# Kernel optimization log

Hardware: AMD Instinct MI355X
Metric: run time of the kernel (lower is better)

## Reference

```python
import jax, jax.numpy as jnp
import numpy as np

D_MODEL = 1024
HIDDEN = 64
N_STEPS = 6
T0, T1 = 0.0, 1.0


def setup_inputs() -> dict:
    key = jax.random.key(0)
    kx, k1, k2, k3, k4 = jax.random.split(key, 5)
    # PyTorch nn.Linear default init: U(-1/sqrt(fan_in), 1/sqrt(fan_in))
    s1 = 1.0 / np.sqrt(D_MODEL + 1)
    s2 = 1.0 / np.sqrt(HIDDEN)
    return {
        "x": jax.random.normal(kx, (8, 2048, D_MODEL), dtype=jnp.float32),
        "W1": jax.random.uniform(k1, (D_MODEL + 1, HIDDEN), jnp.float32, -s1, s1),
        "b1": jax.random.uniform(k2, (HIDDEN,), jnp.float32, -s1, s1),
        "W2": jax.random.uniform(k3, (HIDDEN, D_MODEL), jnp.float32, -s2, s2),
        "b2": jax.random.uniform(k4, (D_MODEL,), jnp.float32, -s2, s2),
    }


def _dynamics(t, z, W1, b1, W2, b2):
    # Equivalent to concat([z, t*ones], -1) @ W1: split the last row of W1
    # (the time channel) so we avoid materializing the concat.
    h = jnp.tanh(jnp.einsum("btd,dh->bth", z, W1[:-1]) + t * W1[-1] + b1)
    return jnp.einsum("bth,hd->btd", h, W2) + b2


def reference(x, W1, b1, W2, b2):
    h = (T1 - T0) / N_STEPS  # step size
    ts = T0 + h * jnp.arange(N_STEPS, dtype=x.dtype)

    def rk4_step(z, t):
        k1 = _dynamics(t, z, W1, b1, W2, b2)
        k2 = _dynamics(t + h / 2, z + (h / 2) * k1, W1, b1, W2, b2)
        k3 = _dynamics(t + h / 2, z + (h / 2) * k2, W1, b1, W2, b2)
        k4 = _dynamics(t + h, z + h * k3, W1, b1, W2, b2)
        z_next = z + (h / 6) * (k1 + 2 * k2 + 2 * k3 + k4)
        return z_next, None

    z_T, _ = jax.lax.scan(rk4_step, x, ts)
    return z_T
```

## Files before the change

### kernel.cpp

```cpp
#include <hip/hip_runtime.h>
#include <hip/hip_bf16.h>

#define DM 1024
#define HID 64
#define NSTEP 6
#define RSTEP (1.0f/6.0f)

using short8  = __attribute__((ext_vector_type(8))) short;
using short4v = __attribute__((ext_vector_type(4))) short;
using f32x4   = __attribute__((ext_vector_type(4))) float;

#define WS_W1P 0
#define WS_W2P 131072
#define WS_GP  262144
#define WS_U   270336

#define L_H0 0
#define L_H1 2304
#define L_HB 4608
#define L_B2 6912
#define LDS_TOTAL 11008
#define HP 144

#define BAR() asm volatile("s_waitcnt lgkmcnt(0)\n\ts_barrier" ::: "memory")

__device__ __forceinline__ short f2bf(float f) {
    __hip_bfloat16 h = __float2bfloat16(f);
    short s;
    __builtin_memcpy(&s, &h, 2);
    return s;
}
__device__ __forceinline__ float ftanh(float x) {
    x = fminf(fmaxf(x, -10.f), 10.f);
    float e = __expf(2.f * x);
    return __fdividef(e - 1.f, e + 1.f);
}

__global__ void k_prep(const float* __restrict__ W1, const float* __restrict__ W2,
                       const float* __restrict__ b2,
                       short* __restrict__ W1P, short* __restrict__ W2P,
                       short* __restrict__ GP, float* __restrict__ U) {
    __shared__ float red[4][64];
    int b = blockIdx.x;
    int t = threadIdx.x;
    int l = t & 63, q4 = t >> 6;
    if (b < 128) {
        if (t < 64) {
            int kk = b >> 2, c = b & 3;
            int col = c * 16 + (l & 15);
            int kb = kk * 32 + ((l >> 4) << 3);
            short8 v;
            #pragma unroll
            for (int i = 0; i < 8; ++i) v[i] = f2bf(W1[(kb + i) * HID + col]);
            *(short8*)(W1P + (((kk * 4 + c) * 64) + l) * 8) = v;
        }
    } else if (b < 256) {
        if (t < 64) {
            int bb = b - 128;
            int kk2 = bb >> 6, ct = bb & 63;
            int col = ct * 16 + (l & 15);
            int kb = kk2 * 32 + ((l >> 4) << 3);
            short8 v;
            #pragma unroll
            for (int i = 0; i < 8; ++i) v[i] = f2bf(W2[(kb + i) * DM + col]);
            *(short8*)(W2P + (((kk2 * 64 + ct) * 64) + l) * 8) = v;
        }
    } else if (b < 320) {
        int j = b - 256;
        float acc = 0.f;
        #pragma unroll 8
        for (int d = q4 * 256; d < q4 * 256 + 256; ++d)
            acc += W2[j * DM + d] * W1[d * HID + l];
        red[q4][l] = acc;
        __syncthreads();
        if (t < 64) {
            float a = red[0][l] + red[1][l] + red[2][l] + red[3][l];
            int kk = j >> 5, lk = (j >> 3) & 3, ii = j & 7, c = l >> 4, lo = l & 15;
            GP[(((kk * 4 + c) * 64) + lk * 16 + lo) * 8 + ii] = f2bf(a);
        }
    } else {
        float acc = 0.f;
        #pragma unroll 8
        for (int d = q4 * 256; d < q4 * 256 + 256; ++d)
            acc += b2[d] * W1[d * HID + l];
        red[q4][l] = acc;
        __syncthreads();
        if (t < 64) U[l] = red[0][l] + red[1][l] + red[2][l] + red[3][l];
    }
}

__global__ __launch_bounds__(256) __attribute__((amdgpu_waves_per_eu(2, 4)))
void k_ode(
        const float* __restrict__ X, const float* __restrict__ W1,
        const float* __restrict__ b1, const float* __restrict__ b2,
        const short* __restrict__ W1P, const short* __restrict__ W2P,
        const short* __restrict__ GP, const float* __restrict__ U,
        float* __restrict__ OUT) {
    extern __shared__ char smem[];
    const int t = threadIdx.x;
    const int lane = t & 63;
    const int w = t >> 6;
    const int hq = lane >> 4;
    const int l15 = lane & 15;
    const int hcol0 = w * 16 + hq * 4;
    const size_t row0 = (size_t)blockIdx.x * 16;

    *(f32x4*)(smem + L_B2 + t * 16) = *(const f32x4*)(b2 + t * 4);

    f32x4 u4   = *(const f32x4*)(U + hcol0);
    f32x4 b14  = *(const f32x4*)(b1 + hcol0);
    f32x4 w1t4 = *(const f32x4*)(W1 + DM * HID + hcol0);
    short8 gf0 = *(const short8*)(GP + (w * 64 + lane) * 8);
    short8 gf1 = *(const short8*)(GP + ((4 + w) * 64 + lane) * 8);

    f32x4 sz;
    {
        const float* xrow = X + (row0 + l15) * DM;
        const short8* wp = (const short8*)W1P + (w * 64 + lane);
        f32x4 a0 = (f32x4){0.f, 0.f, 0.f, 0.f};
        f32x4 a1 = (f32x4){0.f, 0.f, 0.f, 0.f};
        #pragma unroll 4
        for (int kk = 0; kk < 32; kk += 2) {
            const float* xp = xrow + (kk << 5) + (hq << 3);
            f32x4 lo0 = *(const f32x4*)(xp);
            f32x4 hi0 = *(const f32x4*)(xp + 4);
            f32x4 lo1 = *(const f32x4*)(xp + 32);
            f32x4 hi1 = *(const f32x4*)(xp + 36);
            short8 zf0, zf1;
            #pragma unroll
            for (int j = 0; j < 4; ++j) {
                zf0[j] = f2bf(lo0[j]); zf0[4 + j] = f2bf(hi0[j]);
                zf1[j] = f2bf(lo1[j]); zf1[4 + j] = f2bf(hi1[j]);
            }
            a0 = __builtin_amdgcn_mfma_f32_16x16x32_bf16(wp[kk * 256],       zf0, a0, 0, 0, 0);
            a1 = __builtin_amdgcn_mfma_f32_16x16x32_bf16(wp[(kk + 1) * 256], zf1, a1, 0, 0, 0);
        }
        sz = a0 + a1;
    }

    f32x4 ssum = (f32x4){0.f, 0.f, 0.f, 0.f};

    for (int s = 0; s < NSTEP; ++s) {
        const float tcur = RSTEP * (float)s;

        f32x4 hsum;
        {
            short4v hc;
            #pragma unroll
            for (int j = 0; j < 4; ++j) {
                float T = sz[j] + tcur * w1t4[j] + b14[j];
                float h = ftanh(T);
                hsum[j] = h;
                hc[j] = f2bf(h);
            }
            *(short4v*)(smem + L_H0 + l15 * HP + hcol0 * 2) = hc;
        }
        BAR();

        #pragma unroll
        for (int st = 0; st < 3; ++st) {
            const float c_i = (st == 2) ? RSTEP : (0.5f * RSTEP);
            const float t_i = tcur + ((st == 2) ? RSTEP : (0.5f * RSTEP));
            const float w_i = (st == 2) ? 1.f : 2.f;
            const int rbuf = (st & 1) ? L_H1 : L_H0;
            const int wbuf = (st & 1) ? L_H0 : L_H1;

            short8 hf0 = *(const short8*)(smem + rbuf + l15 * HP + (hq << 4));
            short8 hf1 = *(const short8*)(smem + rbuf + l15 * HP + 64 + (hq << 4));
            f32x4 dd = (f32x4){0.f, 0.f, 0.f, 0.f};
            dd = __builtin_amdgcn_mfma_f32_16x16x32_bf16(gf0, hf0, dd, 0, 0, 0);
            dd = __builtin_amdgcn_mfma_f32_16x16x32_bf16(gf1, hf1, dd, 0, 0, 0);
            short4v hc;
            #pragma unroll
            for (int j = 0; j < 4; ++j) {
                float T = sz[j] + c_i * (dd[j] + u4[j]) + t_i * w1t4[j] + b14[j];
                float h = ftanh(T);
                hsum[j] += w_i * h;
                hc[j] = f2bf(h);
            }
            if (st < 2) {
                *(short4v*)(smem + wbuf + l15 * HP + hcol0 * 2) = hc;
            } else {
                short4v hb4;
                #pragma unroll
                for (int j = 0; j < 4; ++j) {
                    ssum[j] += hsum[j] * (RSTEP / 6.f);
                    hb4[j] = (s < NSTEP - 1) ? f2bf(hsum[j] * (RSTEP / 6.f))
                                             : f2bf(ssum[j]);
                }
                *(short4v*)(smem + L_HB + l15 * HP + hcol0 * 2) = hb4;
            }
            BAR();
        }

        if (s < NSTEP - 1) {
            short8 hb0 = *(const short8*)(smem + L_HB + l15 * HP + (hq << 4));
            short8 hb1 = *(const short8*)(smem + L_HB + l15 * HP + 64 + (hq << 4));
            f32x4 d = (f32x4){0.f, 0.f, 0.f, 0.f};
            d = __builtin_amdgcn_mfma_f32_16x16x32_bf16(gf0, hb0, d, 0, 0, 0);
            d = __builtin_amdgcn_mfma_f32_16x16x32_bf16(gf1, hb1, d, 0, 0, 0);
            #pragma unroll
            for (int j = 0; j < 4; ++j)
                sz[j] += d[j] + RSTEP * u4[j];
        }
    }

    {
        short8 sb0 = *(const short8*)(smem + L_HB + l15 * HP + (hq << 4));
        short8 sb1 = *(const short8*)(smem + L_HB + l15 * HP + 64 + (hq << 4));
        const short8* w2p8 = (const short8*)W2P;
        const float* xrow = X + (row0 + l15) * DM + w * 256;
        float* orow = OUT + (row0 + l15) * DM + w * 256;
        #pragma unroll 4
        for (int q = 0; q < 16; ++q) {
            int ct = w * 16 + q;
            short8 wa = w2p8[ct * 64 + lane];
            short8 wb = w2p8[(64 + ct) * 64 + lane];
            f32x4 p = (f32x4){0.f, 0.f, 0.f, 0.f};
            p = __builtin_amdgcn_mfma_f32_16x16x32_bf16(wa, sb0, p, 0, 0, 0);
            p = __builtin_amdgcn_mfma_f32_16x16x32_bf16(wb, sb1, p, 0, 0, 0);
            f32x4 b2v = *(const f32x4*)(smem + L_B2 + (ct * 16 + hq * 4) * 4);
            f32x4 xv  = *(const f32x4*)(xrow + q * 16 + hq * 4);
            f32x4 nv;
            #pragma unroll
            for (int j = 0; j < 4; ++j)
                nv[j] = xv[j] + p[j] + b2v[j];
            *(f32x4*)(orow + q * 16 + hq * 4) = nv;
        }
    }
}

extern "C" void kernel_launch(void* const* d_in, const int* in_sizes, int n_in,
                              void* d_out, int out_size, void* d_ws, size_t ws_size,
                              hipStream_t stream) {
    (void)in_sizes; (void)n_in; (void)out_size; (void)ws_size;
    const float* X  = (const float*)d_in[0];
    const float* W1 = (const float*)d_in[1];
    const float* b1 = (const float*)d_in[2];
    const float* W2 = (const float*)d_in[3];
    const float* b2 = (const float*)d_in[4];
    float* OUT = (float*)d_out;
    short* W1P = (short*)((char*)d_ws + WS_W1P);
    short* W2P = (short*)((char*)d_ws + WS_W2P);
    short* GP  = (short*)((char*)d_ws + WS_GP);
    float* U   = (float*)((char*)d_ws + WS_U);

    k_prep<<<321, 256, 0, stream>>>(W1, W2, b2, W1P, W2P, GP, U);
    k_ode<<<1024, 256, LDS_TOTAL, stream>>>(X, W1, b1, b2, W1P, W2P, GP, U, OUT);
}
```

Before: 78.51 us.

## Use single-wave blocks to drop barriers and precompute per-stage bias vectors

Shrinks each ODE block from four waves to one. The single wave now owns all 64 hidden columns across four MFMA tiles, so the workgroup barriers between RK4 stages reduce to LDS waitcnt fences and one LDS buffer replaces the two ping-pong buffers plus the separate sum buffer. The prep kernel also precomputes per-step, per-stage constant vectors (b1 + t*w1t + c*u) and h*u, which removes per-element arithmetic from the inner loop. In exchange, each wave holds more register state and does four times the serial MFMA and global-load work, and only 1024 single-wave blocks remain to fill the device. That may reduce latency hiding.

```diff
diff --git a/kernel.cpp b/kernel.cpp
--- a/kernel.cpp
+++ b/kernel.cpp
@@ -14,15 +14,16 @@
 #define WS_W2P 131072
 #define WS_GP  262144
 #define WS_U   270336
-
-#define L_H0 0
-#define L_H1 2304
-#define L_HB 4608
-#define L_B2 6912
-#define LDS_TOTAL 11008
+#define WS_VST 270592
+#define WS_HU  276736
+
+#define L_H   0
+#define L_VST 2304
+#define L_HU  8448
+#define LDS_TOTAL 8704
 #define HP 144
 
-#define BAR() asm volatile("s_waitcnt lgkmcnt(0)\n\ts_barrier" ::: "memory")
+#define FENCE() asm volatile("s_waitcnt lgkmcnt(0)" ::: "memory")
 
 __device__ __forceinline__ short f2bf(float f) {
     __hip_bfloat16 h = __float2bfloat16(f);
@@ -37,9 +38,10 @@
 }
 
 __global__ void k_prep(const float* __restrict__ W1, const float* __restrict__ W2,
-                       const float* __restrict__ b2,
+                       const float* __restrict__ b1, const float* __restrict__ b2,
                        short* __restrict__ W1P, short* __restrict__ W2P,
-                       short* __restrict__ GP, float* __restrict__ U) {
+                       short* __restrict__ GP, float* __restrict__ U,
+                       float* __restrict__ VST, float* __restrict__ HU) {
     __shared__ float red[4][64];
     int b = blockIdx.x;
     int t = threadIdx.x;
@@ -85,147 +87,158 @@
             acc += b2[d] * W1[d * HID + l];
         red[q4][l] = acc;
         __syncthreads();
-        if (t < 64) U[l] = red[0][l] + red[1][l] + red[2][l] + red[3][l];
-    }
-}
-
-__global__ __launch_bounds__(256) __attribute__((amdgpu_waves_per_eu(2, 4)))
+        if (t < 64) {
+            float uu = red[0][l] + red[1][l] + red[2][l] + red[3][l];
+            U[l] = uu;
+            HU[l] = RSTEP * uu;
+            float b1l = b1[l];
+            float wtl = W1[DM * HID + l];
+            #pragma unroll
+            for (int s6 = 0; s6 < 6; ++s6) {
+                float ts = RSTEP * (float)s6;
+                float tm = ts + 0.5f * RSTEP;
+                float vmid = b1l + tm * wtl + 0.5f * RSTEP * uu;
+                VST[(s6 * 4 + 0) * 64 + l] = b1l + ts * wtl;
+                VST[(s6 * 4 + 1) * 64 + l] = vmid;
+                VST[(s6 * 4 + 2) * 64 + l] = vmid;
+                VST[(s6 * 4 + 3) * 64 + l] = b1l + (ts + RSTEP) * wtl + RSTEP * uu;
+            }
+        }
+    }
+}
+
+__global__ __launch_bounds__(64) __attribute__((amdgpu_waves_per_eu(2, 4)))
 void k_ode(
-        const float* __restrict__ X, const float* __restrict__ W1,
-        const float* __restrict__ b1, const float* __restrict__ b2,
+        const float* __restrict__ X, const float* __restrict__ b2,
         const short* __restrict__ W1P, const short* __restrict__ W2P,
-        const short* __restrict__ GP, const float* __restrict__ U,
-        float* __restrict__ OUT) {
+        const short* __restrict__ GP, const float* __restrict__ VST,
+        const float* __restrict__ HU, float* __restrict__ OUT) {
     extern __shared__ char smem[];
-    const int t = threadIdx.x;
-    const int lane = t & 63;
-    const int w = t >> 6;
+    const int lane = threadIdx.x & 63;
     const int hq = lane >> 4;
     const int l15 = lane & 15;
-    const int hcol0 = w * 16 + hq * 4;
     const size_t row0 = (size_t)blockIdx.x * 16;
-
-    *(f32x4*)(smem + L_B2 + t * 16) = *(const f32x4*)(b2 + t * 4);
-
-    f32x4 u4   = *(const f32x4*)(U + hcol0);
-    f32x4 b14  = *(const f32x4*)(b1 + hcol0);
-    f32x4 w1t4 = *(const f32x4*)(W1 + DM * HID + hcol0);
-    short8 gf0 = *(const short8*)(GP + (w * 64 + lane) * 8);
-    short8 gf1 = *(const short8*)(GP + ((4 + w) * 64 + lane) * 8);
-
-    f32x4 sz;
+    const float* xrow = X + (row0 + l15) * DM;
+
+    #pragma unroll
+    for (int i = 0; i < 6; ++i)
+        *(f32x4*)(smem + L_VST + i * 1024 + lane * 16) =
+            *(const f32x4*)(VST + i * 256 + lane * 4);
+    if (lane < 16)
+        *(f32x4*)(smem + L_HU + lane * 16) = *(const f32x4*)(HU + lane * 4);
+
+    short8 gfr[2][4];
+    #pragma unroll
+    for (int k2 = 0; k2 < 2; ++k2)
+        #pragma unroll
+        for (int c = 0; c < 4; ++c)
+            gfr[k2][c] = *(const short8*)(GP + ((k2 * 4 + c) * 64 + lane) * 8);
+
+    f32x4 sz[4] = {(f32x4){0.f,0.f,0.f,0.f}, (f32x4){0.f,0.f,0.f,0.f},
+                   (f32x4){0.f,0.f,0.f,0.f}, (f32x4){0.f,0.f,0.f,0.f}};
     {
-        const float* xrow = X + (row0 + l15) * DM;
-        const short8* wp = (const short8*)W1P + (w * 64 + lane);
-        f32x4 a0 = (f32x4){0.f, 0.f, 0.f, 0.f};
-        f32x4 a1 = (f32x4){0.f, 0.f, 0.f, 0.f};
+        const short8* wp = (const short8*)W1P;
         #pragma unroll 4
-        for (int kk = 0; kk < 32; kk += 2) {
+        for (int kk = 0; kk < 32; ++kk) {
             const float* xp = xrow + (kk << 5) + (hq << 3);
-            f32x4 lo0 = *(const f32x4*)(xp);
-            f32x4 hi0 = *(const f32x4*)(xp + 4);
-            f32x4 lo1 = *(const f32x4*)(xp + 32);
-            f32x4 hi1 = *(const f32x4*)(xp + 36);
-            short8 zf0, zf1;
+            f32x4 lo = *(const f32x4*)(xp);
+            f32x4 hi = *(const f32x4*)(xp + 4);
+            short8 zf;
+            #pragma unroll
+            for (int j = 0; j < 4; ++j) { zf[j] = f2bf(lo[j]); zf[4 + j] = f2bf(hi[j]); }
+            #pragma unroll
+            for (int c = 0; c < 4; ++c)
+                sz[c] = __builtin_amdgcn_mfma_f32_16x16x32_bf16(
+                            wp[(kk * 4 + c) * 64 + lane], zf, sz[c], 0, 0, 0);
+        }
+    }
+
+    f32x4 ssum[4] = {(f32x4){0.f,0.f,0.f,0.f}, (f32x4){0.f,0.f,0.f,0.f},
+                     (f32x4){0.f,0.f,0.f,0.f}, (f32x4){0.f,0.f,0.f,0.f}};
+
+    for (int s = 0; s < NSTEP; ++s) {
+        f32x4 hsum[4];
+
+        #pragma unroll
+        for (int c = 0; c < 4; ++c) {
+            f32x4 vst = *(const f32x4*)(smem + L_VST + (s * 4 + 0) * 256 + c * 64 + (hq << 4));
+            short4v hc;
             #pragma unroll
             for (int j = 0; j < 4; ++j) {
-                zf0[j] = f2bf(lo0[j]); zf0[4 + j] = f2bf(hi0[j]);
-                zf1[j] = f2bf(lo1[j]); zf1[4 + j] = f2bf(hi1[j]);
-            }
-            a0 = __builtin_amdgcn_mfma_f32_16x16x32_bf16(wp[kk * 256],       zf0, a0, 0, 0, 0);
-            a1 = __builtin_amdgcn_mfma_f32_16x16x32_bf16(wp[(kk + 1) * 256], zf1, a1, 0, 0, 0);
-        }
-        sz = a0 + a1;
-    }
-
-    f32x4 ssum = (f32x4){0.f, 0.f, 0.f, 0.f};
-
-    for (int s = 0; s < NSTEP; ++s) {
-        const float tcur = RSTEP * (float)s;
-
-        f32x4 hsum;
-        {
-            short4v hc;
-            #pragma unroll
-            for (int j = 0; j < 4; ++j) {
-                float T = sz[j] + tcur * w1t4[j] + b14[j];
-                float h = ftanh(T);
-                hsum[j] = h;
+                float h = ftanh(sz[c][j] + vst[j]);
+                hsum[c][j] = h;
                 hc[j] = f2bf(h);
             }
-            *(short4v*)(smem + L_H0 + l15 * HP + hcol0 * 2) = hc;
-        }
-        BAR();
+            *(short4v*)(smem + L_H + l15 * HP + c * 32 + (hq << 3)) = hc;
+        }
+        FENCE();
 
         #pragma unroll
-        for (int st = 0; st < 3; ++st) {
-            const float c_i = (st == 2) ? RSTEP : (0.5f * RSTEP);
-            const float t_i = tcur + ((st == 2) ? RSTEP : (0.5f * RSTEP));
-            const float w_i = (st == 2) ? 1.f : 2.f;
-            const int rbuf = (st & 1) ? L_H1 : L_H0;
-            const int wbuf = (st & 1) ? L_H0 : L_H1;
-
-            short8 hf0 = *(const short8*)(smem + rbuf + l15 * HP + (hq << 4));
-            short8 hf1 = *(const short8*)(smem + rbuf + l15 * HP + 64 + (hq << 4));
-            f32x4 dd = (f32x4){0.f, 0.f, 0.f, 0.f};
-            dd = __builtin_amdgcn_mfma_f32_16x16x32_bf16(gf0, hf0, dd, 0, 0, 0);
-            dd = __builtin_amdgcn_mfma_f32_16x16x32_bf16(gf1, hf1, dd, 0, 0, 0);
-            short4v hc;
-            #pragma unroll
-            for (int j = 0; j < 4; ++j) {
-                float T = sz[j] + c_i * (dd[j] + u4[j]) + t_i * w1t4[j] + b14[j];
-                float h = ftanh(T);
-                hsum[j] += w_i * h;
-                hc[j] = f2bf(h);
-            }
-            if (st < 2) {
-                *(short4v*)(smem + wbuf + l15 * HP + hcol0 * 2) = hc;
-            } else {
-                short4v hb4;
+        for (int e = 1; e < 4; ++e) {
+            const float ce = (e == 3) ? RSTEP : (0.5f * RSTEP);
+            const float we = (e == 3) ? 1.f : 2.f;
+            short8 hf0 = *(const short8*)(smem + L_H + l15 * HP + (hq << 4));
+            short8 hf1 = *(const short8*)(smem + L_H + l15 * HP + 64 + (hq << 4));
+            #pragma unroll
+            for (int c = 0; c < 4; ++c) {
+                f32x4 dd = (f32x4){0.f, 0.f, 0.f, 0.f};
+                dd = __builtin_amdgcn_mfma_f32_16x16x32_bf16(gfr[0][c], hf0, dd, 0, 0, 0);
+                dd = __builtin_amdgcn_mfma_f32_16x16x32_bf16(gfr[1][c], hf1, dd, 0, 0, 0);
+                f32x4 vst = *(const f32x4*)(smem + L_VST + (s * 4 + e) * 256 + c * 64 + (hq << 4));
+                short4v hc;
                 #pragma unroll
                 for (int j = 0; j < 4; ++j) {
-                    ssum[j] += hsum[j] * (RSTEP / 6.f);
-                    hb4[j] = (s < NSTEP - 1) ? f2bf(hsum[j] * (RSTEP / 6.f))
-                                             : f2bf(ssum[j]);
+                    float h = ftanh(sz[c][j] + ce * dd[j] + vst[j]);
+                    hsum[c][j] += we * h;
+                    if (e < 3) {
+                        hc[j] = f2bf(h);
+                    } else {
+                        ssum[c][j] += hsum[c][j] * (RSTEP / 6.f);
+                        hc[j] = (s < NSTEP - 1) ? f2bf(hsum[c][j] * (RSTEP / 6.f))
+                                                : f2bf(ssum[c][j]);
+                    }
                 }
-                *(short4v*)(smem + L_HB + l15 * HP + hcol0 * 2) = hb4;
-            }
-            BAR();
+                *(short4v*)(smem + L_H + l15 * HP + c * 32 + (hq << 3)) = hc;
+            }
+            FENCE();
         }
 
         if (s < NSTEP - 1) {
-            short8 hb0 = *(const short8*)(smem + L_HB + l15 * HP + (hq << 4));
-            short8 hb1 = *(const short8*)(smem + L_HB + l15 * HP + 64 + (hq << 4));
-            f32x4 d = (f32x4){0.f, 0.f, 0.f, 0.f};
-            d = __builtin_amdgcn_mfma_f32_16x16x32_bf16(gf0, hb0, d, 0, 0, 0);
-            d = __builtin_amdgcn_mfma_f32_16x16x32_bf16(gf1, hb1, d, 0, 0, 0);
-            #pragma unroll
-            for (int j = 0; j < 4; ++j)
-                sz[j] += d[j] + RSTEP * u4[j];
+            short8 hb0 = *(const short8*)(smem + L_H + l15 * HP + (hq << 4));
+            short8 hb1 = *(const short8*)(smem + L_H + l15 * HP + 64 + (hq << 4));
+            #pragma unroll
+            for (int c = 0; c < 4; ++c) {
+                f32x4 d = (f32x4){0.f, 0.f, 0.f, 0.f};
+                d = __builtin_amdgcn_mfma_f32_16x16x32_bf16(gfr[0][c], hb0, d, 0, 0, 0);
+                d = __builtin_amdgcn_mfma_f32_16x16x32_bf16(gfr[1][c], hb1, d, 0, 0, 0);
+                f32x4 hu4 = *(const f32x4*)(smem + L_HU + c * 64 + (hq << 4));
+                #pragma unroll
+                for (int j = 0; j < 4; ++j)
+                    sz[c][j] += d[j] + hu4[j];
+            }
         }
     }
 
     {
-        short8 sb0 = *(const short8*)(smem + L_HB + l15 * HP + (hq << 4));
-        short8 sb1 = *(const short8*)(smem + L_HB + l15 * HP + 64 + (hq << 4));
+        short8 sb0 = *(const short8*)(smem + L_H + l15 * HP + (hq << 4));
+        short8 sb1 = *(const short8*)(smem + L_H + l15 * HP + 64 + (hq << 4));
         const short8* w2p8 = (const short8*)W2P;
-        const float* xrow = X + (row0 + l15) * DM + w * 256;
-        float* orow = OUT + (row0 + l15) * DM + w * 256;
+        float* orow = OUT + (row0 + l15) * DM;
         #pragma unroll 4
-        for (int q = 0; q < 16; ++q) {
-            int ct = w * 16 + q;
+        for (int ct = 0; ct < 64; ++ct) {
             short8 wa = w2p8[ct * 64 + lane];
             short8 wb = w2p8[(64 + ct) * 64 + lane];
             f32x4 p = (f32x4){0.f, 0.f, 0.f, 0.f};
             p = __builtin_amdgcn_mfma_f32_16x16x32_bf16(wa, sb0, p, 0, 0, 0);
             p = __builtin_amdgcn_mfma_f32_16x16x32_bf16(wb, sb1, p, 0, 0, 0);
-            f32x4 b2v = *(const f32x4*)(smem + L_B2 + (ct * 16 + hq * 4) * 4);
-            f32x4 xv  = *(const f32x4*)(xrow + q * 16 + hq * 4);
+            int col = ct * 16 + (hq << 2);
+            f32x4 xv  = *(const f32x4*)(xrow + col);
+            f32x4 b2v = *(const f32x4*)(b2 + col);
             f32x4 nv;
             #pragma unroll
             for (int j = 0; j < 4; ++j)
                 nv[j] = xv[j] + p[j] + b2v[j];
-            *(f32x4*)(orow + q * 16 + hq * 4) = nv;
+            *(f32x4*)(orow + col) = nv;
         }
     }
 }
@@ -244,7 +257,9 @@
     short* W2P = (short*)((char*)d_ws + WS_W2P);
     short* GP  = (short*)((char*)d_ws + WS_GP);
     float* U   = (float*)((char*)d_ws + WS_U);
-
-    k_prep<<<321, 256, 0, stream>>>(W1, W2, b2, W1P, W2P, GP, U);
-    k_ode<<<1024, 256, LDS_TOTAL, stream>>>(X, W1, b1, b2, W1P, W2P, GP, U, OUT);
-}
+    float* VST = (float*)((char*)d_ws + WS_VST);
+    float* HU  = (float*)((char*)d_ws + WS_HU);
+
+    k_prep<<<321, 256, 0, stream>>>(W1, W2, b1, b2, W1P, W2P, GP, U, VST, HU);
+    k_ode<<<1024, 64, LDS_TOTAL, stream>>>(X, b2, W1P, W2P, GP, VST, HU, OUT);
+}
```

Result: slower. 84.27 us (+7.3%).
